# Performance work log

Measured on AMD Instinct MI355X. Metric: run time of the kernel, lower is better.

The kernel has to match this reference:

```python
import jax, jax.numpy as jnp
import numpy as np
import math

J = 50000      # number of atomic environments
NSP = 4        # number of species
NMAX = 8       # max radial
LMAX = 6       # max angular


def setup_inputs() -> dict:
    key = jax.random.key(0)
    keys = jax.random.split(key, LMAX + 1)
    inp = {}
    for l in range(LMAX + 1):
        inp[f"se_{l}"] = jax.random.normal(keys[l], (J, NSP, NMAX, 2 * l + 1), dtype=jnp.float32)
    return inp


def _powerspectrum(se_list):
    Jn, nsp, nmax, _ = se_list[0].shape
    A = nsp * nmax
    diag_ids = np.arange(A)
    iu0, iu1 = np.triu_indices(A, k=1)
    parts = []
    for l, se in enumerate(se_list):
        se = se.reshape(Jn, A, 2 * l + 1)
        # symmetric Gram over the combined (species, radial) channel, contracted over m
        outer = jnp.einsum('iam,ibm->iab', se, se) / math.sqrt(2 * l + 1)  # [J, A, A]
        diag = outer[:, diag_ids, diag_ids]                # [J, A]
        upper = math.sqrt(2.0) * outer[:, iu0, iu1]        # [J, A*(A-1)/2]
        parts.append(jnp.concatenate([diag, upper], axis=1))
    # concatenating per-l blocks in order l=0..lmax matches PS.view(J, -1)
    return jnp.concatenate(parts, axis=1)


def reference(se_0, se_1, se_2, se_3, se_4, se_5, se_6):
    se_list = [se_0, se_1, se_2, se_3, se_4, se_5, se_6]
    ps = _powerspectrum(se_list)                           # [J, D]
    # torch.nn.functional.normalize(..., dim=1): x / max(||x||_2, 1e-12)
    norm = jnp.linalg.norm(ps, axis=1, keepdims=True)
    return ps / jnp.maximum(norm, 1e-12)
```

## Files before the change

kernel.cpp:

```cpp
#include <hip/hip_runtime.h>

#define NL 7
#define NA 32
#define PERL 528
#define NF 3696
#define RSH 24
#define SQRT2f 1.41421356237309515f

typedef short bf16x8 __attribute__((ext_vector_type(8)));
typedef float f32x16 __attribute__((ext_vector_type(16)));
typedef unsigned uint4v __attribute__((ext_vector_type(4)));
typedef float f32x4u __attribute__((ext_vector_type(4), aligned(4)));

__device__ __forceinline__ unsigned cvtpk(float lo, float hi) {
    unsigned r;
    asm("v_cvt_pk_bf16_f32 %0, %1, %2" : "=v"(r) : "v"(lo), "v"(hi));
    return r;
}

template<int L>
__device__ __forceinline__ void stage_lo(const float* __restrict__ se, int j, int a,
                                         unsigned short* __restrict__ Th) {
    constexpr int m21 = 2 * L + 1;
    const float* rowp = se + (size_t)j * (32 * m21) + a * m21;
    float v[8];
    #pragma unroll
    for (int i = 0; i < 8; ++i) v[i] = 0.0f;
    if constexpr (m21 == 1) { v[0] = rowp[0]; }
    else if constexpr (m21 == 3) {
        f32x4u t = *(const f32x4u*)rowp;
        v[0] = t[0]; v[1] = t[1]; v[2] = t[2];
    } else if constexpr (m21 == 5) {
        f32x4u t = *(const f32x4u*)rowp;
        v[0] = t[0]; v[1] = t[1]; v[2] = t[2]; v[3] = t[3];
        v[4] = rowp[4];
    } else {
        f32x4u t0 = *(const f32x4u*)rowp;
        f32x4u t1 = *(const f32x4u*)(rowp + 3);
        v[0] = t0[0]; v[1] = t0[1]; v[2] = t0[2];
        v[3] = t1[0]; v[4] = t1[1]; v[5] = t1[2]; v[6] = t1[3];
    }
    unsigned pk[4];
    #pragma unroll
    for (int p = 0; p < 4; ++p) pk[p] = (2 * p < m21) ? cvtpk(v[2 * p], v[2 * p + 1]) : 0u;
    unsigned short* rp = Th + (L * 32 + a) * RSH;
    *(uint4*)rp       = make_uint4(pk[0], pk[1], pk[2], pk[3]);
    *(uint4*)(rp + 8) = make_uint4(0u, 0u, 0u, 0u);
}

template<int L>
__device__ __forceinline__ void stage_hi(const float* __restrict__ se, int j, int a,
                                         unsigned short* __restrict__ Th) {
    constexpr int m21 = 2 * L + 1;
    const float* rowp = se + (size_t)j * (32 * m21) + a * m21;
    float v[16];
    #pragma unroll
    for (int i = 0; i < 16; ++i) v[i] = 0.0f;
    {
        f32x4u t0 = *(const f32x4u*)rowp;
        f32x4u t1 = *(const f32x4u*)(rowp + 4);
        #pragma unroll
        for (int i = 0; i < 4; ++i) { v[i] = t0[i]; v[4 + i] = t1[i]; }
    }
    if constexpr (m21 == 9) { v[8] = rowp[8]; }
    else if constexpr (m21 == 11) {
        f32x4u t = *(const f32x4u*)(rowp + 7);
        v[8] = t[1]; v[9] = t[2]; v[10] = t[3];
    } else {
        f32x4u t = *(const f32x4u*)(rowp + 8);
        v[8] = t[0]; v[9] = t[1]; v[10] = t[2]; v[11] = t[3];
        v[12] = rowp[12];
    }
    unsigned pk[8];
    #pragma unroll
    for (int p = 0; p < 8; ++p) pk[p] = (2 * p < m21) ? cvtpk(v[2 * p], v[2 * p + 1]) : 0u;
    unsigned short* rp = Th + (L * 32 + a) * RSH;
    *(uint4*)rp       = make_uint4(pk[0], pk[1], pk[2], pk[3]);
    *(uint4*)(rp + 8) = make_uint4(pk[4], pk[5], pk[6], pk[7]);
}

__global__ __launch_bounds__(256) void ps_kernel(
    const float* __restrict__ se0, const float* __restrict__ se1,
    const float* __restrict__ se2, const float* __restrict__ se3,
    const float* __restrict__ se4, const float* __restrict__ se5,
    const float* __restrict__ se6, float* __restrict__ out)
{
    __shared__ __align__(16) float LB[NF];
    __shared__ float s_wsum[4];
    unsigned short* Th = (unsigned short*)LB;

    const int j    = blockIdx.x;
    const int tid  = threadIdx.x;
    const int wv   = tid >> 6;
    const int lane = tid & 63;

    {
        const int a = lane & 31;
        if (lane < 32) {
            switch (wv) {
                case 0:  stage_lo<0>(se0, j, a, Th); break;
                case 1:  stage_lo<1>(se1, j, a, Th); break;
                case 2:  stage_lo<2>(se2, j, a, Th); break;
                default: stage_lo<3>(se3, j, a, Th); break;
            }
        } else {
            switch (wv) {
                case 0:  stage_hi<4>(se4, j, a, Th); break;
                case 1:  stage_hi<5>(se5, j, a, Th); break;
                case 2:  stage_hi<6>(se6, j, a, Th); break;
                default: break;
            }
        }
    }
    __builtin_amdgcn_wave_barrier();
    asm volatile("" ::: "memory");

    const int row  = lane & 31;
    const int hoff = (lane >> 5) * 8;
    const int lA = wv;
    const int lB = wv + 4;

    f32x16 accA, accB;
    #pragma unroll
    for (int r = 0; r < 16; ++r) { accA[r] = 0.0f; accB[r] = 0.0f; }

    {
        const bf16x8 fA = *(const bf16x8*)(Th + (lA * 32 + row) * RSH + hoff);
        accA = __builtin_amdgcn_mfma_f32_32x32x16_bf16(fA, fA, accA, 0, 0, 0);
    }
    if (lB < NL) {
        const bf16x8 fB = *(const bf16x8*)(Th + (lB * 32 + row) * RSH + hoff);
        accB = __builtin_amdgcn_mfma_f32_32x32x16_bf16(fB, fB, accB, 0, 0, 0);
    }

    const float rsA = rsqrtf((float)(2 * lA + 1));
    const float rsB = rsqrtf((float)(2 * lB + 1));
    float sA = 0.0f, sB = 0.0f;
    #pragma unroll
    for (int r = 0; r < 16; ++r) { sA += accA[r] * accA[r]; sB += accB[r] * accB[r]; }
    float ssq = sA * (rsA * rsA) + ((lB < NL) ? sB * (rsB * rsB) : 0.0f);

    #pragma unroll
    for (int off = 32; off >= 1; off >>= 1) ssq += __shfl_down(ssq, off, 64);
    if (lane == 0) s_wsum[wv] = ssq;
    __syncthreads();

    const float tot = s_wsum[0] + s_wsum[1] + s_wsum[2] + s_wsum[3];
    const float inv = 1.0f / fmaxf(sqrtf(tot), 1e-12f);

    const int c     = lane & 31;
    const int hi4   = (lane >> 5) * 4;
    const int ubase = 32 + (c * (63 - c)) / 2 - c - 1;

    {
        const float dsc = rsA * inv, usc = dsc * SQRT2f;
        float* ol = LB + lA * PERL;
        #pragma unroll
        for (int r = 0; r < 16; ++r) {
            const int rw = (r & 3) + 8 * (r >> 2) + hi4;
            if (rw >= c) {
                const bool d = (rw == c);
                ol[d ? c : (ubase + rw)] = accA[r] * (d ? dsc : usc);
            }
        }
    }
    if (lB < NL) {
        const float dsc = rsB * inv, usc = dsc * SQRT2f;
        float* ol = LB + lB * PERL;
        #pragma unroll
        for (int r = 0; r < 16; ++r) {
            const int rw = (r & 3) + 8 * (r >> 2) + hi4;
            if (rw >= c) {
                const bool d = (rw == c);
                ol[d ? c : (ubase + rw)] = accB[r] * (d ? dsc : usc);
            }
        }
    }
    __syncthreads();

    const uint4v* ob4 = (const uint4v*)LB;
    uint4v* op4 = (uint4v*)(out + (size_t)j * NF);
    #pragma unroll
    for (int k = 0; k < 4; ++k) {
        const int q = tid + k * 256;
        if (q < 924) {
            uint4v v = ob4[q];
            __builtin_nontemporal_store(v, &op4[q]);
        }
    }
}

extern "C" void kernel_launch(void* const* d_in, const int* in_sizes, int n_in,
                              void* d_out, int out_size, void* d_ws, size_t ws_size,
                              hipStream_t stream) {
    const float* se0 = (const float*)d_in[0];
    const float* se1 = (const float*)d_in[1];
    const float* se2 = (const float*)d_in[2];
    const float* se3 = (const float*)d_in[3];
    const float* se4 = (const float*)d_in[4];
    const float* se5 = (const float*)d_in[5];
    const float* se6 = (const float*)d_in[6];
    float* out = (float*)d_out;

    const int J = in_sizes[0] / NA;
    ps_kernel<<<J, 256, 0, stream>>>(se0, se1, se2, se3, se4, se5, se6, out);
}
```

Measured before the change: 198.5 us.

## Use one wave per angular channel with 512-thread blocks

The block grows from 4 to 8 waves, so each of the 7 angular channels gets its own wave. That wave stages its bf16 tile with both half-waves (the two 8-wide m halves), runs a single MFMA, and writes its own triangle. This removes the per-wave double MFMA and the idle-lane imbalance of the previous lo/hi split, and adds more threads for the output store. In exchange the block is larger, has one fully idle wave, and the launch-bounds occupancy hint changes.

```diff
diff --git a/kernel.cpp b/kernel.cpp
--- a/kernel.cpp
+++ b/kernel.cpp
@@ -19,74 +19,80 @@
 }
 
 template<int L>
-__device__ __forceinline__ void stage_lo(const float* __restrict__ se, int j, int a,
-                                         unsigned short* __restrict__ Th) {
+__device__ __forceinline__ f32x16 process(const float* __restrict__ se, int j,
+                                          int lane, unsigned short* __restrict__ Th) {
     constexpr int m21 = 2 * L + 1;
+    const int a = lane & 31;
+    const int h = lane >> 5;
     const float* rowp = se + (size_t)j * (32 * m21) + a * m21;
-    float v[8];
+
+    unsigned pk[4] = {0u, 0u, 0u, 0u};
+    if (h == 0) {
+        float v[8];
+        #pragma unroll
+        for (int i = 0; i < 8; ++i) v[i] = 0.0f;
+        if constexpr (m21 >= 8) {
+            f32x4u t0 = *(const f32x4u*)rowp;
+            f32x4u t1 = *(const f32x4u*)(rowp + 4);
+            #pragma unroll
+            for (int i = 0; i < 4; ++i) { v[i] = t0[i]; v[4 + i] = t1[i]; }
+        } else if constexpr (m21 == 1) {
+            v[0] = rowp[0];
+        } else if constexpr (m21 == 3) {
+            f32x4u t = *(const f32x4u*)rowp;
+            v[0] = t[0]; v[1] = t[1]; v[2] = t[2];
+        } else if constexpr (m21 == 5) {
+            f32x4u t = *(const f32x4u*)rowp;
+            v[0] = t[0]; v[1] = t[1]; v[2] = t[2]; v[3] = t[3];
+            v[4] = rowp[4];
+        } else {
+            f32x4u t0 = *(const f32x4u*)rowp;
+            f32x4u t1 = *(const f32x4u*)(rowp + 3);
+            v[0] = t0[0]; v[1] = t0[1]; v[2] = t0[2];
+            v[3] = t1[0]; v[4] = t1[1]; v[5] = t1[2]; v[6] = t1[3];
+        }
+        #pragma unroll
+        for (int p = 0; p < 4; ++p)
+            if (2 * p < m21) pk[p] = cvtpk(v[2 * p], v[2 * p + 1]);
+    } else if constexpr (m21 > 8) {
+        float v[8];
+        #pragma unroll
+        for (int i = 0; i < 8; ++i) v[i] = 0.0f;
+        if constexpr (m21 == 9) {
+            v[0] = rowp[8];
+        } else if constexpr (m21 == 11) {
+            f32x4u t = *(const f32x4u*)(rowp + 7);
+            v[0] = t[1]; v[1] = t[2]; v[2] = t[3];
+        } else {
+            f32x4u t = *(const f32x4u*)(rowp + 8);
+            v[0] = t[0]; v[1] = t[1]; v[2] = t[2]; v[3] = t[3];
+            v[4] = rowp[12];
+        }
+        #pragma unroll
+        for (int p = 0; p < 4; ++p)
+            if (8 + 2 * p < m21) pk[p] = cvtpk(v[2 * p], v[2 * p + 1]);
+    }
+    unsigned short* rp = Th + (L * 32 + a) * RSH + 8 * h;
+    *(uint4*)rp = make_uint4(pk[0], pk[1], pk[2], pk[3]);
+
+    __builtin_amdgcn_wave_barrier();
+    asm volatile("" ::: "memory");
+
+    const bf16x8 f = *(const bf16x8*)(Th + (L * 32 + (lane & 31)) * RSH + (lane >> 5) * 8);
+    f32x16 z;
     #pragma unroll
-    for (int i = 0; i < 8; ++i) v[i] = 0.0f;
-    if constexpr (m21 == 1) { v[0] = rowp[0]; }
-    else if constexpr (m21 == 3) {
-        f32x4u t = *(const f32x4u*)rowp;
-        v[0] = t[0]; v[1] = t[1]; v[2] = t[2];
-    } else if constexpr (m21 == 5) {
-        f32x4u t = *(const f32x4u*)rowp;
-        v[0] = t[0]; v[1] = t[1]; v[2] = t[2]; v[3] = t[3];
-        v[4] = rowp[4];
-    } else {
-        f32x4u t0 = *(const f32x4u*)rowp;
-        f32x4u t1 = *(const f32x4u*)(rowp + 3);
-        v[0] = t0[0]; v[1] = t0[1]; v[2] = t0[2];
-        v[3] = t1[0]; v[4] = t1[1]; v[5] = t1[2]; v[6] = t1[3];
-    }
-    unsigned pk[4];
-    #pragma unroll
-    for (int p = 0; p < 4; ++p) pk[p] = (2 * p < m21) ? cvtpk(v[2 * p], v[2 * p + 1]) : 0u;
-    unsigned short* rp = Th + (L * 32 + a) * RSH;
-    *(uint4*)rp       = make_uint4(pk[0], pk[1], pk[2], pk[3]);
-    *(uint4*)(rp + 8) = make_uint4(0u, 0u, 0u, 0u);
+    for (int r = 0; r < 16; ++r) z[r] = 0.0f;
+    return __builtin_amdgcn_mfma_f32_32x32x16_bf16(f, f, z, 0, 0, 0);
 }
 
-template<int L>
-__device__ __forceinline__ void stage_hi(const float* __restrict__ se, int j, int a,
-                                         unsigned short* __restrict__ Th) {
-    constexpr int m21 = 2 * L + 1;
-    const float* rowp = se + (size_t)j * (32 * m21) + a * m21;
-    float v[16];
-    #pragma unroll
-    for (int i = 0; i < 16; ++i) v[i] = 0.0f;
-    {
-        f32x4u t0 = *(const f32x4u*)rowp;
-        f32x4u t1 = *(const f32x4u*)(rowp + 4);
-        #pragma unroll
-        for (int i = 0; i < 4; ++i) { v[i] = t0[i]; v[4 + i] = t1[i]; }
-    }
-    if constexpr (m21 == 9) { v[8] = rowp[8]; }
-    else if constexpr (m21 == 11) {
-        f32x4u t = *(const f32x4u*)(rowp + 7);
-        v[8] = t[1]; v[9] = t[2]; v[10] = t[3];
-    } else {
-        f32x4u t = *(const f32x4u*)(rowp + 8);
-        v[8] = t[0]; v[9] = t[1]; v[10] = t[2]; v[11] = t[3];
-        v[12] = rowp[12];
-    }
-    unsigned pk[8];
-    #pragma unroll
-    for (int p = 0; p < 8; ++p) pk[p] = (2 * p < m21) ? cvtpk(v[2 * p], v[2 * p + 1]) : 0u;
-    unsigned short* rp = Th + (L * 32 + a) * RSH;
-    *(uint4*)rp       = make_uint4(pk[0], pk[1], pk[2], pk[3]);
-    *(uint4*)(rp + 8) = make_uint4(pk[4], pk[5], pk[6], pk[7]);
-}
-
-__global__ __launch_bounds__(256) void ps_kernel(
+__global__ __launch_bounds__(512, 8) void ps_kernel(
     const float* __restrict__ se0, const float* __restrict__ se1,
     const float* __restrict__ se2, const float* __restrict__ se3,
     const float* __restrict__ se4, const float* __restrict__ se5,
     const float* __restrict__ se6, float* __restrict__ out)
 {
     __shared__ __align__(16) float LB[NF];
-    __shared__ float s_wsum[4];
+    __shared__ float s_wsum[8];
     unsigned short* Th = (unsigned short*)LB;
 
     const int j    = blockIdx.x;
@@ -94,85 +100,48 @@
     const int wv   = tid >> 6;
     const int lane = tid & 63;
 
-    {
-        const int a = lane & 31;
-        if (lane < 32) {
-            switch (wv) {
-                case 0:  stage_lo<0>(se0, j, a, Th); break;
-                case 1:  stage_lo<1>(se1, j, a, Th); break;
-                case 2:  stage_lo<2>(se2, j, a, Th); break;
-                default: stage_lo<3>(se3, j, a, Th); break;
-            }
-        } else {
-            switch (wv) {
-                case 0:  stage_hi<4>(se4, j, a, Th); break;
-                case 1:  stage_hi<5>(se5, j, a, Th); break;
-                case 2:  stage_hi<6>(se6, j, a, Th); break;
-                default: break;
-            }
-        }
-    }
-    __builtin_amdgcn_wave_barrier();
-    asm volatile("" ::: "memory");
-
-    const int row  = lane & 31;
-    const int hoff = (lane >> 5) * 8;
-    const int lA = wv;
-    const int lB = wv + 4;
-
-    f32x16 accA, accB;
+    f32x16 acc;
     #pragma unroll
-    for (int r = 0; r < 16; ++r) { accA[r] = 0.0f; accB[r] = 0.0f; }
-
-    {
-        const bf16x8 fA = *(const bf16x8*)(Th + (lA * 32 + row) * RSH + hoff);
-        accA = __builtin_amdgcn_mfma_f32_32x32x16_bf16(fA, fA, accA, 0, 0, 0);
-    }
-    if (lB < NL) {
-        const bf16x8 fB = *(const bf16x8*)(Th + (lB * 32 + row) * RSH + hoff);
-        accB = __builtin_amdgcn_mfma_f32_32x32x16_bf16(fB, fB, accB, 0, 0, 0);
+    for (int r = 0; r < 16; ++r) acc[r] = 0.0f;
+    switch (wv) {
+        case 0: acc = process<0>(se0, j, lane, Th); break;
+        case 1: acc = process<1>(se1, j, lane, Th); break;
+        case 2: acc = process<2>(se2, j, lane, Th); break;
+        case 3: acc = process<3>(se3, j, lane, Th); break;
+        case 4: acc = process<4>(se4, j, lane, Th); break;
+        case 5: acc = process<5>(se5, j, lane, Th); break;
+        case 6: acc = process<6>(se6, j, lane, Th); break;
+        default: break;
     }
 
-    const float rsA = rsqrtf((float)(2 * lA + 1));
-    const float rsB = rsqrtf((float)(2 * lB + 1));
-    float sA = 0.0f, sB = 0.0f;
+    const float rs = rsqrtf((float)(2 * wv + 1));
+    float ssq = 0.0f;
     #pragma unroll
-    for (int r = 0; r < 16; ++r) { sA += accA[r] * accA[r]; sB += accB[r] * accB[r]; }
-    float ssq = sA * (rsA * rsA) + ((lB < NL) ? sB * (rsB * rsB) : 0.0f);
+    for (int r = 0; r < 16; ++r) ssq += acc[r] * acc[r];
+    ssq *= rs * rs;
 
     #pragma unroll
     for (int off = 32; off >= 1; off >>= 1) ssq += __shfl_down(ssq, off, 64);
     if (lane == 0) s_wsum[wv] = ssq;
     __syncthreads();
 
-    const float tot = s_wsum[0] + s_wsum[1] + s_wsum[2] + s_wsum[3];
+    float tot = 0.0f;
+    #pragma unroll
+    for (int w = 0; w < 8; ++w) tot += s_wsum[w];
     const float inv = 1.0f / fmaxf(sqrtf(tot), 1e-12f);
 
-    const int c     = lane & 31;
-    const int hi4   = (lane >> 5) * 4;
-    const int ubase = 32 + (c * (63 - c)) / 2 - c - 1;
-
-    {
-        const float dsc = rsA * inv, usc = dsc * SQRT2f;
-        float* ol = LB + lA * PERL;
+    if (wv < NL) {
+        const int c     = lane & 31;
+        const int hi4   = (lane >> 5) * 4;
+        const int ubase = 32 + (c * (63 - c)) / 2 - c - 1;
+        const float dsc = rs * inv, usc = dsc * SQRT2f;
+        float* ol = LB + wv * PERL;
         #pragma unroll
         for (int r = 0; r < 16; ++r) {
             const int rw = (r & 3) + 8 * (r >> 2) + hi4;
             if (rw >= c) {
                 const bool d = (rw == c);
-                ol[d ? c : (ubase + rw)] = accA[r] * (d ? dsc : usc);
-            }
-        }
-    }
-    if (lB < NL) {
-        const float dsc = rsB * inv, usc = dsc * SQRT2f;
-        float* ol = LB + lB * PERL;
-        #pragma unroll
-        for (int r = 0; r < 16; ++r) {
-            const int rw = (r & 3) + 8 * (r >> 2) + hi4;
-            if (rw >= c) {
-                const bool d = (rw == c);
-                ol[d ? c : (ubase + rw)] = accB[r] * (d ? dsc : usc);
+                ol[d ? c : (ubase + rw)] = acc[r] * (d ? dsc : usc);
             }
         }
     }
@@ -181,8 +150,8 @@
     const uint4v* ob4 = (const uint4v*)LB;
     uint4v* op4 = (uint4v*)(out + (size_t)j * NF);
     #pragma unroll
-    for (int k = 0; k < 4; ++k) {
-        const int q = tid + k * 256;
+    for (int k = 0; k < 2; ++k) {
+        const int q = tid + k * 512;
         if (q < 924) {
             uint4v v = ob4[q];
             __builtin_nontemporal_store(v, &op4[q]);
@@ -203,5 +172,5 @@
     float* out = (float*)d_out;
 
     const int J = in_sizes[0] / NA;
-    ps_kernel<<<J, 256, 0, stream>>>(se0, se1, se2, se3, se4, se5, se6, out);
+    ps_kernel<<<J, 512, 0, stream>>>(se0, se1, se2, se3, se4, se5, se6, out);
 }
```

Measured after the change: 209.6 us. 5.6% more time.

## Use persistent blocks with register double-buffered prefetch of next environment

Applied to the files above, without the earlier changes.

Launches a fixed grid of 2000 persistent blocks. Each block loops over environments with a stride, loading the next environment's raw inputs into registers while the current one is staged, multiplied by MFMA, normalized and stored. The aim is to hide global load latency and cut block launch overhead. In exchange it adds an extra barrier per iteration and more register pressure, and a fixed grid size may under- or over-subscribe the CUs.

```diff
diff --git a/kernel.cpp b/kernel.cpp
--- a/kernel.cpp
+++ b/kernel.cpp
@@ -1,10 +1,10 @@
 #include <hip/hip_runtime.h>
 
 #define NL 7
-#define NA 32
 #define PERL 528
 #define NF 3696
 #define RSH 24
+#define NB 2000
 #define SQRT2f 1.41421356237309515f
 
 typedef short bf16x8 __attribute__((ext_vector_type(8)));
@@ -18,62 +18,59 @@
     return r;
 }
 
-template<int L>
-__device__ __forceinline__ void stage_lo(const float* __restrict__ se, int j, int a,
-                                         unsigned short* __restrict__ Th) {
+__device__ __forceinline__ void block_barrier_lds() {
+    asm volatile("s_waitcnt lgkmcnt(0)" ::: "memory");
+    __builtin_amdgcn_s_barrier();
+    __builtin_amdgcn_sched_barrier(0);
+}
+
+template<int L, bool HI>
+__device__ __forceinline__ void load_raw(const float* __restrict__ se, int j, int a, f32x16& v) {
     constexpr int m21 = 2 * L + 1;
     const float* rowp = se + (size_t)j * (32 * m21) + a * m21;
-    float v[8];
-    #pragma unroll
-    for (int i = 0; i < 8; ++i) v[i] = 0.0f;
-    if constexpr (m21 == 1) { v[0] = rowp[0]; }
-    else if constexpr (m21 == 3) {
-        f32x4u t = *(const f32x4u*)rowp;
-        v[0] = t[0]; v[1] = t[1]; v[2] = t[2];
-    } else if constexpr (m21 == 5) {
-        f32x4u t = *(const f32x4u*)rowp;
-        v[0] = t[0]; v[1] = t[1]; v[2] = t[2]; v[3] = t[3];
-        v[4] = rowp[4];
+    if constexpr (!HI) {
+        if constexpr (m21 == 1) { v[0] = rowp[0]; }
+        else if constexpr (m21 == 3) {
+            f32x4u t = *(const f32x4u*)rowp;
+            v[0] = t[0]; v[1] = t[1]; v[2] = t[2];
+        } else if constexpr (m21 == 5) {
+            f32x4u t = *(const f32x4u*)rowp;
+            v[0] = t[0]; v[1] = t[1]; v[2] = t[2]; v[3] = t[3];
+            v[4] = rowp[4];
+        } else {
+            f32x4u t0 = *(const f32x4u*)rowp;
+            f32x4u t1 = *(const f32x4u*)(rowp + 3);
+            v[0] = t0[0]; v[1] = t0[1]; v[2] = t0[2];
+            v[3] = t1[0]; v[4] = t1[1]; v[5] = t1[2]; v[6] = t1[3];
+        }
     } else {
         f32x4u t0 = *(const f32x4u*)rowp;
-        f32x4u t1 = *(const f32x4u*)(rowp + 3);
-        v[0] = t0[0]; v[1] = t0[1]; v[2] = t0[2];
-        v[3] = t1[0]; v[4] = t1[1]; v[5] = t1[2]; v[6] = t1[3];
+        f32x4u t1 = *(const f32x4u*)(rowp + 4);
+        #pragma unroll
+        for (int i = 0; i < 4; ++i) { v[i] = t0[i]; v[4 + i] = t1[i]; }
+        if constexpr (m21 == 9) { v[8] = rowp[8]; }
+        else if constexpr (m21 == 11) {
+            f32x4u t = *(const f32x4u*)(rowp + 7);
+            v[8] = t[1]; v[9] = t[2]; v[10] = t[3];
+        } else {
+            f32x4u t = *(const f32x4u*)(rowp + 8);
+            v[8] = t[0]; v[9] = t[1]; v[10] = t[2]; v[11] = t[3];
+            v[12] = rowp[12];
+        }
     }
-    unsigned pk[4];
-    #pragma unroll
-    for (int p = 0; p < 4; ++p) pk[p] = (2 * p < m21) ? cvtpk(v[2 * p], v[2 * p + 1]) : 0u;
-    unsigned short* rp = Th + (L * 32 + a) * RSH;
-    *(uint4*)rp       = make_uint4(pk[0], pk[1], pk[2], pk[3]);
-    *(uint4*)(rp + 8) = make_uint4(0u, 0u, 0u, 0u);
 }
 
 template<int L>
-__device__ __forceinline__ void stage_hi(const float* __restrict__ se, int j, int a,
-                                         unsigned short* __restrict__ Th) {
+__device__ __forceinline__ void stage_row(int a, const f32x16& v, unsigned short* Th) {
     constexpr int m21 = 2 * L + 1;
-    const float* rowp = se + (size_t)j * (32 * m21) + a * m21;
-    float v[16];
-    #pragma unroll
-    for (int i = 0; i < 16; ++i) v[i] = 0.0f;
-    {
-        f32x4u t0 = *(const f32x4u*)rowp;
-        f32x4u t1 = *(const f32x4u*)(rowp + 4);
-        #pragma unroll
-        for (int i = 0; i < 4; ++i) { v[i] = t0[i]; v[4 + i] = t1[i]; }
-    }
-    if constexpr (m21 == 9) { v[8] = rowp[8]; }
-    else if constexpr (m21 == 11) {
-        f32x4u t = *(const f32x4u*)(rowp + 7);
-        v[8] = t[1]; v[9] = t[2]; v[10] = t[3];
-    } else {
-        f32x4u t = *(const f32x4u*)(rowp + 8);
-        v[8] = t[0]; v[9] = t[1]; v[10] = t[2]; v[11] = t[3];
-        v[12] = rowp[12];
-    }
     unsigned pk[8];
     #pragma unroll
-    for (int p = 0; p < 8; ++p) pk[p] = (2 * p < m21) ? cvtpk(v[2 * p], v[2 * p + 1]) : 0u;
+    for (int p = 0; p < 8; ++p) {
+        if constexpr (false) {}
+        if (2 * p + 1 < m21)    pk[p] = cvtpk(v[2 * p], v[2 * p + 1]);
+        else if (2 * p < m21)   pk[p] = cvtpk(v[2 * p], 0.0f);
+        else                    pk[p] = 0u;
+    }
     unsigned short* rp = Th + (L * 32 + a) * RSH;
     *(uint4*)rp       = make_uint4(pk[0], pk[1], pk[2], pk[3]);
     *(uint4*)(rp + 8) = make_uint4(pk[4], pk[5], pk[6], pk[7]);
@@ -83,110 +80,142 @@
     const float* __restrict__ se0, const float* __restrict__ se1,
     const float* __restrict__ se2, const float* __restrict__ se3,
     const float* __restrict__ se4, const float* __restrict__ se5,
-    const float* __restrict__ se6, float* __restrict__ out)
+    const float* __restrict__ se6, float* __restrict__ out, int J)
 {
     __shared__ __align__(16) float LB[NF];
     __shared__ float s_wsum[4];
     unsigned short* Th = (unsigned short*)LB;
 
-    const int j    = blockIdx.x;
     const int tid  = threadIdx.x;
     const int wv   = tid >> 6;
     const int lane = tid & 63;
-
-    {
-        const int a = lane & 31;
-        if (lane < 32) {
-            switch (wv) {
-                case 0:  stage_lo<0>(se0, j, a, Th); break;
-                case 1:  stage_lo<1>(se1, j, a, Th); break;
-                case 2:  stage_lo<2>(se2, j, a, Th); break;
-                default: stage_lo<3>(se3, j, a, Th); break;
-            }
-        } else {
-            switch (wv) {
-                case 0:  stage_hi<4>(se4, j, a, Th); break;
-                case 1:  stage_hi<5>(se5, j, a, Th); break;
-                case 2:  stage_hi<6>(se6, j, a, Th); break;
-                default: break;
-            }
-        }
-    }
-    __builtin_amdgcn_wave_barrier();
-    asm volatile("" ::: "memory");
-
-    const int row  = lane & 31;
-    const int hoff = (lane >> 5) * 8;
-    const int lA = wv;
-    const int lB = wv + 4;
-
-    f32x16 accA, accB;
-    #pragma unroll
-    for (int r = 0; r < 16; ++r) { accA[r] = 0.0f; accB[r] = 0.0f; }
-
-    {
-        const bf16x8 fA = *(const bf16x8*)(Th + (lA * 32 + row) * RSH + hoff);
-        accA = __builtin_amdgcn_mfma_f32_32x32x16_bf16(fA, fA, accA, 0, 0, 0);
-    }
-    if (lB < NL) {
-        const bf16x8 fB = *(const bf16x8*)(Th + (lB * 32 + row) * RSH + hoff);
-        accB = __builtin_amdgcn_mfma_f32_32x32x16_bf16(fB, fB, accB, 0, 0, 0);
-    }
-
-    const float rsA = rsqrtf((float)(2 * lA + 1));
-    const float rsB = rsqrtf((float)(2 * lB + 1));
-    float sA = 0.0f, sB = 0.0f;
-    #pragma unroll
-    for (int r = 0; r < 16; ++r) { sA += accA[r] * accA[r]; sB += accB[r] * accB[r]; }
-    float ssq = sA * (rsA * rsA) + ((lB < NL) ? sB * (rsB * rsB) : 0.0f);
-
-    #pragma unroll
-    for (int off = 32; off >= 1; off >>= 1) ssq += __shfl_down(ssq, off, 64);
-    if (lane == 0) s_wsum[wv] = ssq;
-    __syncthreads();
-
-    const float tot = s_wsum[0] + s_wsum[1] + s_wsum[2] + s_wsum[3];
-    const float inv = 1.0f / fmaxf(sqrtf(tot), 1e-12f);
-
+    const int a    = lane & 31;
+    const bool hi  = lane >= 32;
+
+    int j = blockIdx.x;
+    if (j >= J) return;
+
+    const float rsA = rsqrtf((float)(2 * wv + 1));
+    const float rsB = rsqrtf((float)(2 * wv + 9));
+    const int row   = lane & 31;
+    const int hoff  = (lane >> 5) * 8;
     const int c     = lane & 31;
     const int hi4   = (lane >> 5) * 4;
     const int ubase = 32 + (c * (63 - c)) / 2 - c - 1;
 
-    {
-        const float dsc = rsA * inv, usc = dsc * SQRT2f;
-        float* ol = LB + lA * PERL;
-        #pragma unroll
-        for (int r = 0; r < 16; ++r) {
-            const int rw = (r & 3) + 8 * (r >> 2) + hi4;
-            if (rw >= c) {
-                const bool d = (rw == c);
-                ol[d ? c : (ubase + rw)] = accA[r] * (d ? dsc : usc);
-            }
-        }
-    }
-    if (lB < NL) {
-        const float dsc = rsB * inv, usc = dsc * SQRT2f;
-        float* ol = LB + lB * PERL;
-        #pragma unroll
-        for (int r = 0; r < 16; ++r) {
-            const int rw = (r & 3) + 8 * (r >> 2) + hi4;
-            if (rw >= c) {
-                const bool d = (rw == c);
-                ol[d ? c : (ubase + rw)] = accB[r] * (d ? dsc : usc);
-            }
-        }
-    }
-    __syncthreads();
-
-    const uint4v* ob4 = (const uint4v*)LB;
-    uint4v* op4 = (uint4v*)(out + (size_t)j * NF);
-    #pragma unroll
-    for (int k = 0; k < 4; ++k) {
-        const int q = tid + k * 256;
-        if (q < 924) {
-            uint4v v = ob4[q];
-            __builtin_nontemporal_store(v, &op4[q]);
-        }
+    auto loadv = [&](f32x16& v, int jj) {
+        if (!hi) {
+            switch (wv) {
+                case 0:  load_raw<0, false>(se0, jj, a, v); break;
+                case 1:  load_raw<1, false>(se1, jj, a, v); break;
+                case 2:  load_raw<2, false>(se2, jj, a, v); break;
+                default: load_raw<3, false>(se3, jj, a, v); break;
+            }
+        } else {
+            switch (wv) {
+                case 0:  load_raw<4, true>(se4, jj, a, v); break;
+                case 1:  load_raw<5, true>(se5, jj, a, v); break;
+                case 2:  load_raw<6, true>(se6, jj, a, v); break;
+                default: break;
+            }
+        }
+    };
+
+    auto process = [&](const f32x16& v, int jj) {
+        if (!hi) {
+            switch (wv) {
+                case 0:  stage_row<0>(a, v, Th); break;
+                case 1:  stage_row<1>(a, v, Th); break;
+                case 2:  stage_row<2>(a, v, Th); break;
+                default: stage_row<3>(a, v, Th); break;
+            }
+        } else {
+            switch (wv) {
+                case 0:  stage_row<4>(a, v, Th); break;
+                case 1:  stage_row<5>(a, v, Th); break;
+                case 2:  stage_row<6>(a, v, Th); break;
+                default: break;
+            }
+        }
+        __builtin_amdgcn_wave_barrier();
+        asm volatile("" ::: "memory");
+
+        f32x16 accA, accB;
+        #pragma unroll
+        for (int r = 0; r < 16; ++r) { accA[r] = 0.0f; accB[r] = 0.0f; }
+        {
+            const bf16x8 fA = *(const bf16x8*)(Th + (wv * 32 + row) * RSH + hoff);
+            accA = __builtin_amdgcn_mfma_f32_32x32x16_bf16(fA, fA, accA, 0, 0, 0);
+        }
+        if (wv < 3) {
+            const bf16x8 fB = *(const bf16x8*)(Th + ((wv + 4) * 32 + row) * RSH + hoff);
+            accB = __builtin_amdgcn_mfma_f32_32x32x16_bf16(fB, fB, accB, 0, 0, 0);
+        }
+
+        float sA = 0.0f, sB = 0.0f;
+        #pragma unroll
+        for (int r = 0; r < 16; ++r) { sA += accA[r] * accA[r]; sB += accB[r] * accB[r]; }
+        float ssq = sA * (rsA * rsA) + ((wv < 3) ? sB * (rsB * rsB) : 0.0f);
+        #pragma unroll
+        for (int off = 32; off >= 1; off >>= 1) ssq += __shfl_down(ssq, off, 64);
+        if (lane == 0) s_wsum[wv] = ssq;
+
+        block_barrier_lds();
+
+        const float tot = s_wsum[0] + s_wsum[1] + s_wsum[2] + s_wsum[3];
+        const float inv = 1.0f / fmaxf(sqrtf(tot), 1e-12f);
+
+        {
+            const float dsc = rsA * inv, usc = dsc * SQRT2f;
+            float* ol = LB + wv * PERL;
+            #pragma unroll
+            for (int r = 0; r < 16; ++r) {
+                const int rw = (r & 3) + 8 * (r >> 2) + hi4;
+                if (rw >= c) {
+                    const bool d = (rw == c);
+                    ol[d ? c : (ubase + rw)] = accA[r] * (d ? dsc : usc);
+                }
+            }
+        }
+        if (wv < 3) {
+            const float dsc = rsB * inv, usc = dsc * SQRT2f;
+            float* ol = LB + (wv + 4) * PERL;
+            #pragma unroll
+            for (int r = 0; r < 16; ++r) {
+                const int rw = (r & 3) + 8 * (r >> 2) + hi4;
+                if (rw >= c) {
+                    const bool d = (rw == c);
+                    ol[d ? c : (ubase + rw)] = accB[r] * (d ? dsc : usc);
+                }
+            }
+        }
+
+        block_barrier_lds();
+
+        const uint4v* ob4 = (const uint4v*)LB;
+        uint4v* op4 = (uint4v*)(out + (size_t)jj * NF);
+        #pragma unroll
+        for (int k = 0; k < 4; ++k) {
+            const int q = tid + k * 256;
+            if (q < 924) __builtin_nontemporal_store(ob4[q], &op4[q]);
+        }
+
+        block_barrier_lds();
+    };
+
+    f32x16 vA, vB;
+    loadv(vA, j);
+    while (true) {
+        int jn = j + NB;
+        if (jn < J) loadv(vB, jn);
+        process(vA, j);
+        j = jn;
+        if (j >= J) break;
+        jn = j + NB;
+        if (jn < J) loadv(vA, jn);
+        process(vB, j);
+        j = jn;
+        if (j >= J) break;
     }
 }
 
@@ -202,6 +231,6 @@
     const float* se6 = (const float*)d_in[6];
     float* out = (float*)d_out;
 
-    const int J = in_sizes[0] / NA;
-    ps_kernel<<<J, 256, 0, stream>>>(se0, se1, se2, se3, se4, se5, se6, out);
-}
+    const int J = in_sizes[0] / 32;
+    ps_kernel<<<NB, 256, 0, stream>>>(se0, se1, se2, se3, se4, se5, se6, out, J);
+}
```

Result: slower. 273.5 us (+37.7%).
